# Performance work log

Hardware: AMD Instinct MI355X
Metric: run time of the kernel (lower is better)

Reference implementation:

```python
import jax, jax.numpy as jnp
import numpy as np

B, T, D, H, L, V = 2, 1024, 768, 12, 6, 50257
HS = D // H  # head_size = 64
EPS = 1e-5  # torch LayerNorm default


def _ln(x, g, b):
    m = x.mean(-1, keepdims=True)
    var = ((x - m) ** 2).mean(-1, keepdims=True)
    return (x - m) * jax.lax.rsqrt(var + EPS) * g + b


def setup_inputs() -> dict:
    key = jax.random.key(0)
    ks = jax.random.split(key, 12)
    s = 0.02  # init std per _init_weights
    n = lambda k, shape: jax.random.normal(k, shape, jnp.float32) * s
    return {
        "idx": jax.random.randint(ks[0], (B, T), 0, V),
        "tok_emb": n(ks[1], (V, D)),
        "pos_emb": n(ks[2], (T, D)),
        # per-layer stacked weights; per-head Q/K/V (bias=False in source)
        "wq": n(ks[3], (L, H, D, HS)),
        "wk": n(ks[4], (L, H, D, HS)),
        "wv": n(ks[5], (L, H, D, HS)),
        "wproj": n(ks[6], (L, D, D)),
        "bproj": jnp.zeros((L, D), jnp.float32),
        "w1": n(ks[7], (L, D, 4 * D)),
        "b1": jnp.zeros((L, 4 * D), jnp.float32),
        "w2": n(ks[8], (L, 4 * D, D)),
        "b2": jnp.zeros((L, D), jnp.float32),
        "ln1_g": jnp.ones((L, D), jnp.float32),
        "ln1_b": jnp.zeros((L, D), jnp.float32),
        "ln2_g": jnp.ones((L, D), jnp.float32),
        "ln2_b": jnp.zeros((L, D), jnp.float32),
        "lm_w": n(ks[9], (D, V)),
        "lm_b": jnp.zeros((V,), jnp.float32),
    }


def reference(idx, tok_emb, pos_emb, wq, wk, wv, wproj, bproj, w1, b1, w2,
              b2, ln1_g, ln1_b, ln2_g, ln2_b, lm_w, lm_b):
    x = tok_emb[idx] + pos_emb[None, :, :]  # [B,T,D]
    tril = jnp.tril(jnp.ones((T, T), bool))
    scale = HS ** -0.5  # k.shape[-1] ** -0.5 in source
    for l in range(L):  # small fixed layer count
        # batched per-head QKV (equivalent to the per-head Linear loop + concat)
        q = jnp.einsum('btd,hds->bhts', x, wq[l])
        k = jnp.einsum('btd,hds->bhts', x, wk[l])
        v = jnp.einsum('btd,hds->bhts', x, wv[l])
        wei = jnp.einsum('bhts,bhus->bhtu', q, k) * scale
        wei = jnp.where(tril, wei, -jnp.inf)  # causal forward_mask
        wei = jax.nn.softmax(wei, axis=-1)  # every row has >=1 valid entry
        o = jnp.einsum('bhtu,bhus->bhts', wei, v)
        o = o.transpose(0, 2, 1, 3).reshape(B, T, D)  # concat heads
        sa = o @ wproj[l] + bproj[l]
        x = _ln(x + sa, ln1_g[l], ln1_b[l])  # post-LN as in source
        h = jax.nn.relu(x @ w1[l] + b1[l]) @ w2[l] + b2[l]
        x = _ln(x + h, ln2_g[l], ln2_b[l])
    return x @ lm_w + lm_b  # logits [B,T,V]
```

## Files before the change

### kernel.cpp

```cpp
#include <hip/hip_runtime.h>

#define FLAG_RELU 1
#define FLAG_CAUSAL 2
#define FLAG_OUTF32 4

typedef __attribute__((ext_vector_type(4))) float f32x4;
typedef __attribute__((ext_vector_type(8))) short s16x8;
typedef unsigned short u16;

__device__ __forceinline__ float bf2f(u16 u) {
  union { unsigned int i; float f; } x; x.i = ((unsigned int)u) << 16; return x.f;
}
__device__ __forceinline__ u16 f2bf(float f) {
  union { float f; unsigned int i; } x; x.f = f;
  unsigned int r = (x.i + 0x7fffu + ((x.i >> 16) & 1u)) >> 16;
  return (u16)r;
}

__device__ __forceinline__ void gl_lds16(const u16* g, u16* l) {
  __builtin_amdgcn_global_load_lds(
      (const __attribute__((address_space(1))) unsigned int*)g,
      (__attribute__((address_space(3))) unsigned int*)l, 16, 0, 0);
}

__global__ __launch_bounds__(256) void gemm_bt(
    const u16* __restrict__ A, const u16* __restrict__ Bt, void* __restrict__ Cv,
    int M, int N, int K, int lda, int ldb, int ldc,
    int zdiv, long aS1, long aS2, long bS1, long bS2, long cS1, long cS2,
    const float* __restrict__ bias, float scale, int flags)
{
  __shared__ u16 As[128][32];
  __shared__ u16 Bs[128][32];
  int nx = gridDim.x, ny = gridDim.y;
  int nwg = nx * ny;
  int orig = blockIdx.y * nx + blockIdx.x;
  int q = nwg >> 3, r = nwg & 7;
  int xcd = orig & 7, rest = orig >> 3;
  int wgid = (xcd < r ? xcd * (q + 1) : r * (q + 1) + (xcd - r) * q) + rest;
  int tx = wgid / ny, ty = wgid % ny;

  int z = blockIdx.z;
  int z1 = z / zdiv, z2 = z % zdiv;
  const u16* Ab = A + z1 * aS1 + z2 * aS2 + (long)ty * 128 * lda;
  const u16* Bb = Bt + z1 * bS1 + z2 * bS2 + (long)tx * 128 * ldb;
  long offC = z1 * cS1 + z2 * cS2;
  int tid = threadIdx.x;
  int lane = tid & 63, wave = tid >> 6;
  int wm = (wave >> 1) << 6, wn = (wave & 1) << 6;
  int row0 = tid >> 2, cc = (tid & 3) << 3;
  int fr = lane & 15, fq = (lane >> 4) << 3;
  int m0 = ty * 128, n0 = tx * 128;
  f32x4 acc[4][4] = {};
  bool skip = (flags & FLAG_CAUSAL) && (n0 > m0 + 127);
  if (!skip) {
    const u16* a0p = Ab + (long)row0 * lda + cc;
    const u16* a1p = a0p + 64L * lda;
    const u16* b0p = Bb + (long)row0 * ldb + cc;
    const u16* b1p = b0p + 64L * ldb;
    u16* da0 = &As[0][0] + tid * 8;
    u16* da1 = &As[0][0] + 2048 + tid * 8;
    u16* db0 = &Bs[0][0] + tid * 8;
    u16* db1 = &Bs[0][0] + 2048 + tid * 8;
    for (int k0 = 0; k0 < K; k0 += 32) {
      if (k0) __syncthreads();
      gl_lds16(a0p + k0, da0);
      gl_lds16(a1p + k0, da1);
      gl_lds16(b0p + k0, db0);
      gl_lds16(b1p + k0, db1);
      __syncthreads();
      s16x8 af[4], bfr[4];
#pragma unroll
      for (int i = 0; i < 4; i++) af[i] = *(const s16x8*)&As[wm + i * 16 + fr][fq];
#pragma unroll
      for (int i = 0; i < 4; i++) bfr[i] = *(const s16x8*)&Bs[wn + i * 16 + fr][fq];
#pragma unroll
      for (int mi = 0; mi < 4; mi++)
#pragma unroll
        for (int ni = 0; ni < 4; ni++)
          acc[mi][ni] = __builtin_amdgcn_mfma_f32_16x16x32_bf16(af[mi], bfr[ni], acc[mi][ni], 0, 0, 0);
    }
  }
  int eq = (lane >> 4) << 2;
  float* Cf = (float*)Cv;
  u16* Ch = (u16*)Cv;
#pragma unroll
  for (int ni = 0; ni < 4; ni++) {
    int c = n0 + wn + ni * 16 + fr;
    if (c >= N) continue;
    float bv = bias ? bias[c] : 0.f;
#pragma unroll
    for (int mi = 0; mi < 4; mi++) {
      int rbase = m0 + wm + mi * 16 + eq;
#pragma unroll
      for (int j = 0; j < 4; j++) {
        int r = rbase + j;
        float v = acc[mi][ni][j] * scale + bv;
        if ((flags & FLAG_RELU) && v < 0.f) v = 0.f;
        if ((flags & FLAG_CAUSAL) && c > r) v = -1e30f;
        long idx = offC + (long)r * ldc + c;
        if (flags & FLAG_OUTF32) Cf[idx] = v; else Ch[idx] = f2bf(v);
      }
    }
  }
}

__global__ __launch_bounds__(256) void transpose_f2b(
    const float* __restrict__ src, u16* __restrict__ dst,
    int R, int C, int lds_, int ldd, int Cpad, int zdiv,
    long sS1, long sS2, long dS1, long dS2)
{
  __shared__ u16 tile[32][33];
  int z = blockIdx.z;
  const float* s = src + (z / zdiv) * sS1 + (z % zdiv) * sS2;
  u16* d = dst + (z / zdiv) * dS1 + (z % zdiv) * dS2;
  int c0 = blockIdx.x * 32, r0 = blockIdx.y * 32;
  int tx = threadIdx.x & 31, ty = threadIdx.x >> 5;
#pragma unroll
  for (int i = 0; i < 32; i += 8) {
    int r = r0 + ty + i, c = c0 + tx;
    u16 v = 0;
    if (r < R && c < C) v = f2bf(s[(long)r * lds_ + c]);
    tile[ty + i][tx] = v;
  }
  __syncthreads();
#pragma unroll
  for (int i = 0; i < 32; i += 8) {
    int c = c0 + ty + i, r = r0 + tx;
    if (c < Cpad && r < R) d[(long)c * ldd + r] = tile[tx][ty + i];
  }
}

__global__ __launch_bounds__(256) void transpose_b2b(
    const u16* __restrict__ src, u16* __restrict__ dst,
    int R, int C, int lds_, int ldd, int Cpad, int zdiv,
    long sS1, long sS2, long dS1, long dS2)
{
  __shared__ u16 tile[32][33];
  int z = blockIdx.z;
  const u16* s = src + (z / zdiv) * sS1 + (z % zdiv) * sS2;
  u16* d = dst + (z / zdiv) * dS1 + (z % zdiv) * dS2;
  int c0 = blockIdx.x * 32, r0 = blockIdx.y * 32;
  int tx = threadIdx.x & 31, ty = threadIdx.x >> 5;
#pragma unroll
  for (int i = 0; i < 32; i += 8) {
    int r = r0 + ty + i, c = c0 + tx;
    u16 v = 0;
    if (r < R && c < C) v = s[(long)r * lds_ + c];
    tile[ty + i][tx] = v;
  }
  __syncthreads();
#pragma unroll
  for (int i = 0; i < 32; i += 8) {
    int c = c0 + ty + i, r = r0 + tx;
    if (c < Cpad && r < R) d[(long)c * ldd + r] = tile[tx][ty + i];
  }
}

__global__ __launch_bounds__(256) void softmax_rows(u16* __restrict__ S)
{
  __shared__ float red[8];
  long row = blockIdx.x;
  u16* p = S + row * 1024;
  int tid = threadIdx.x;
  float v[4];
  float mx = -1e30f;
#pragma unroll
  for (int i = 0; i < 4; i++) { v[i] = bf2f(p[tid + i * 256]); mx = fmaxf(mx, v[i]); }
  for (int off = 32; off >= 1; off >>= 1) mx = fmaxf(mx, __shfl_down(mx, off));
  if ((tid & 63) == 0) red[tid >> 6] = mx;
  __syncthreads();
  if (tid == 0) red[4] = fmaxf(fmaxf(red[0], red[1]), fmaxf(red[2], red[3]));
  __syncthreads();
  mx = red[4];
  float sum = 0.f;
#pragma unroll
  for (int i = 0; i < 4; i++) { v[i] = __expf(v[i] - mx); sum += v[i]; }
  for (int off = 32; off >= 1; off >>= 1) sum += __shfl_down(sum, off);
  if ((tid & 63) == 0) red[tid >> 6] = sum;
  __syncthreads();
  if (tid == 0) red[5] = red[0] + red[1] + red[2] + red[3];
  __syncthreads();
  float rs = 1.f / red[5];
#pragma unroll
  for (int i = 0; i < 4; i++) p[tid + i * 256] = f2bf(v[i] * rs);
}

__global__ __launch_bounds__(256) void add_ln(
    float* __restrict__ x, const float* __restrict__ d,
    const float* __restrict__ g, const float* __restrict__ b,
    u16* __restrict__ xb)
{
  __shared__ float red[8];
  long base = blockIdx.x * 768L;
  int tid = threadIdx.x;
  float v[3]; float s = 0.f;
#pragma unroll
  for (int i = 0; i < 3; i++) { int k = tid + i * 256; v[i] = x[base + k] + d[base + k]; s += v[i]; }
  for (int off = 32; off >= 1; off >>= 1) s += __shfl_down(s, off);
  if ((tid & 63) == 0) red[tid >> 6] = s;
  __syncthreads();
  if (tid == 0) red[4] = (red[0] + red[1] + red[2] + red[3]) * (1.f / 768.f);
  __syncthreads();
  float mean = red[4];
  float s2 = 0.f;
#pragma unroll
  for (int i = 0; i < 3; i++) { float t = v[i] - mean; s2 += t * t; }
  for (int off = 32; off >= 1; off >>= 1) s2 += __shfl_down(s2, off);
  if ((tid & 63) == 0) red[tid >> 6] = s2;
  __syncthreads();
  if (tid == 0) red[5] = rsqrtf((red[0] + red[1] + red[2] + red[3]) * (1.f / 768.f) + 1e-5f);
  __syncthreads();
  float rstd = red[5];
#pragma unroll
  for (int i = 0; i < 3; i++) {
    int k = tid + i * 256;
    float y = (v[i] - mean) * rstd * g[k] + b[k];
    x[base + k] = y; xb[base + k] = f2bf(y);
  }
}

__global__ __launch_bounds__(256) void embed_kernel(
    const int* __restrict__ idx, const float* __restrict__ tok, const float* __restrict__ pos,
    float* __restrict__ x, u16* __restrict__ xb)
{
  long row = blockIdx.x;
  int t = (int)(row & 1023);
  long tk = idx[row];
  for (int i = threadIdx.x; i < 768; i += 256) {
    float v = tok[tk * 768 + i] + pos[(long)t * 768 + i];
    x[row * 768 + i] = v;
    xb[row * 768 + i] = f2bf(v);
  }
}

extern "C" void kernel_launch(void* const* d_in, const int* in_sizes, int n_in,
                              void* d_out, int out_size, void* d_ws, size_t ws_size,
                              hipStream_t stream)
{
  const int Bb = 2, T = 1024, D = 768, H = 12, L = 6, V = 50257, HS = 64,
            M = 2048, DFF = 3072, NQ = 2304, VP = 50304;
  const int*   idx     = (const int*)d_in[0];
  const float* tok_emb = (const float*)d_in[1];
  const float* pos_emb = (const float*)d_in[2];
  const float* wq      = (const float*)d_in[3];
  const float* wk      = (const float*)d_in[4];
  const float* wv      = (const float*)d_in[5];
  const float* wproj   = (const float*)d_in[6];
  const float* bproj   = (const float*)d_in[7];
  const float* w1      = (const float*)d_in[8];
  const float* b1      = (const float*)d_in[9];
  const float* w2      = (const float*)d_in[10];
  const float* b2      = (const float*)d_in[11];
  const float* ln1g    = (const float*)d_in[12];
  const float* ln1b    = (const float*)d_in[13];
  const float* ln2g    = (const float*)d_in[14];
  const float* ln2b    = (const float*)d_in[15];
  const float* lmw     = (const float*)d_in[16];
  const float* lmb     = (const float*)d_in[17];
  float* out = (float*)d_out;
  (void)in_sizes; (void)n_in; (void)out_size; (void)ws_size;

  char* ws = (char*)d_ws;
  size_t off = 0;
  auto alloc = [&](size_t bytes) -> char* {
    char* p = ws + off; off += (bytes + 255) & ~(size_t)255; return p;
  };
  u16* wqkv_t  = (u16*)alloc((size_t)L * NQ * D * 2);
  u16* wproj_t = (u16*)alloc((size_t)L * D * D * 2);
  u16* w1_t    = (u16*)alloc((size_t)L * DFF * D * 2);
  u16* w2_t    = (u16*)alloc((size_t)L * D * DFF * 2);
  float* x     = (float*)alloc((size_t)M * D * 4);
  u16* xb      = (u16*)alloc((size_t)M * D * 2);
  char* scratch_base = ws + off;
  u16* qkv     = (u16*)alloc((size_t)M * NQ * 2);
  u16* vt      = (u16*)alloc(((size_t)Bb * H * HS * T + 64 * T) * 2);
  u16* S       = (u16*)alloc((size_t)Bb * H * T * T * 2);
  u16* attn    = (u16*)alloc((size_t)M * D * 2);
  float* tmp   = (float*)alloc((size_t)M * D * 4);
  u16* h1      = (u16*)alloc((size_t)M * DFF * 2);
  u16* lmw_t   = (u16*)scratch_base;

  dim3 blk(256);
  {
    long sS1 = (long)H * D * HS, sS2 = (long)D * HS;
    long dS1 = (long)NQ * D,     dS2 = (long)HS * D;
    transpose_f2b<<<dim3(2, 24, L * H), blk, 0, stream>>>(wq, wqkv_t,                     D, HS, HS, D, HS, H, sS1, sS2, dS1, dS2);
    transpose_f2b<<<dim3(2, 24, L * H), blk, 0, stream>>>(wk, wqkv_t + (size_t)D * D,     D, HS, HS, D, HS, H, sS1, sS2, dS1, dS2);
    transpose_f2b<<<dim3(2, 24, L * H), blk, 0, stream>>>(wv, wqkv_t + (size_t)2 * D * D, D, HS, HS, D, HS, H, sS1, sS2, dS1, dS2);
    transpose_f2b<<<dim3(24, 24, L), blk, 0, stream>>>(wproj, wproj_t, D, D, D, D, D, 1, (long)D * D, 0, (long)D * D, 0);
    transpose_f2b<<<dim3(96, 24, L), blk, 0, stream>>>(w1, w1_t, D, DFF, DFF, D, DFF, 1, (long)D * DFF, 0, (long)DFF * D, 0);
    transpose_f2b<<<dim3(24, 96, L), blk, 0, stream>>>(w2, w2_t, DFF, D, D, DFF, D, 1, (long)DFF * D, 0, (long)D * DFF, 0);
  }
  embed_kernel<<<dim3(M), blk, 0, stream>>>(idx, tok_emb, pos_emb, x, xb);

  for (int l = 0; l < L; l++) {
    gemm_bt<<<dim3(NQ / 128, M / 128, 1), blk, 0, stream>>>(
        xb, wqkv_t + (size_t)l * NQ * D, qkv, M, NQ, D, D, D, NQ,
        1, 0, 0, 0, 0, 0, 0, nullptr, 1.f, 0);
    transpose_b2b<<<dim3(2, 32, Bb * H), blk, 0, stream>>>(
        qkv + 2 * D, vt, T, HS, NQ, T, HS, H,
        (long)T * NQ, (long)HS, (long)H * HS * T, (long)HS * T);
    gemm_bt<<<dim3(T / 128, T / 128, Bb * H), blk, 0, stream>>>(
        qkv, qkv + D, S, T, T, HS, NQ, NQ, T,
        H, (long)T * NQ, (long)HS, (long)T * NQ, (long)HS, (long)H * T * T, (long)T * T,
        nullptr, 0.125f, FLAG_CAUSAL);
    softmax_rows<<<dim3(Bb * H * T), blk, 0, stream>>>(S);
    gemm_bt<<<dim3(1, T / 128, Bb * H), blk, 0, stream>>>(
        S, vt, attn, T, HS, T, T, T, D,
        H, (long)H * T * T, (long)T * T, (long)H * HS * T, (long)HS * T, (long)T * D, (long)HS,
        nullptr, 1.f, 0);
    gemm_bt<<<dim3(D / 128, M / 128, 1), blk, 0, stream>>>(
        attn, wproj_t + (size_t)l * D * D, tmp, M, D, D, D, D, D,
        1, 0, 0, 0, 0, 0, 0, bproj + (size_t)l * D, 1.f, FLAG_OUTF32);
    add_ln<<<dim3(M), blk, 0, stream>>>(x, tmp, ln1g + (size_t)l * D, ln1b + (size_t)l * D, xb);
    gemm_bt<<<dim3(DFF / 128, M / 128, 1), blk, 0, stream>>>(
        xb, w1_t + (size_t)l * DFF * D, h1, M, DFF, D, D, D, DFF,
        1, 0, 0, 0, 0, 0, 0, b1 + (size_t)l * DFF, 1.f, FLAG_RELU);
    gemm_bt<<<dim3(D / 128, M / 128, 1), blk, 0, stream>>>(
        h1, w2_t + (size_t)l * D * DFF, tmp, M, D, DFF, DFF, DFF, D,
        1, 0, 0, 0, 0, 0, 0, b2 + (size_t)l * D, 1.f, FLAG_OUTF32);
    add_ln<<<dim3(M), blk, 0, stream>>>(x, tmp, ln2g + (size_t)l * D, ln2b + (size_t)l * D, xb);
  }
  transpose_f2b<<<dim3(1572, 24, 1), blk, 0, stream>>>(lmw, lmw_t, D, V, V, D, VP, 1, 0, 0, 0, 0);
  gemm_bt<<<dim3(VP / 128, M / 128, 1), blk, 0, stream>>>(
      xb, lmw_t, out, M, V, D, D, D, V,
      1, 0, 0, 0, 0, 0, 0, lmb, 1.f, FLAG_OUTF32);
}
```

Before: 2.521 ms.

## Replace unfused attention with a fused causal flash-attention kernel

Replaces the V transpose, the QK^T GEMM writing a full TxT score matrix, the row softmax and the PV GEMM with a single flash-attention kernel. Each block handles 64 queries of one head, streams 64-key tiles through LDS with online softmax, and skips key tiles above the causal diagonal. This removes the large bf16 score-matrix round trips through global memory and three launches per layer. The trade-off is an unpipelined inner loop with two syncs per tile, a per-element V transpose into LDS, and fairly small blocks.

```diff
diff --git a/kernel.cpp b/kernel.cpp
--- a/kernel.cpp
+++ b/kernel.cpp
@@ -104,6 +104,139 @@
   }
 }
 
+__global__ __launch_bounds__(256) void flash_attn(
+    const u16* __restrict__ qkv, u16* __restrict__ attn)
+{
+  __shared__ u16 QL[4096];
+  __shared__ u16 KL[4096];
+  __shared__ u16 VtL[4096];
+  __shared__ u16 PL[4 * 16 * 72];
+  const int NQ = 2304, D = 768, T = 1024;
+  int qt = blockIdx.x, bh = blockIdx.y;
+  int b = bh / 12, h = bh - b * 12;
+  int q0 = qt * 64;
+  int tid = threadIdx.x;
+  int lane = tid & 63, w = tid >> 6;
+  int fr = lane & 15, g = lane >> 4;
+  int eq = g << 2, fq = g << 3;
+  const u16* base = qkv + (long)(b * T) * NQ + h * 64;
+  const u16* Qg = base + (long)q0 * NQ;
+  const u16* Kg = base + 768;
+  const u16* Vg = base + 1536;
+  int srow = tid >> 2, scol = (tid & 3) << 3;
+  int hs0 = (tid & 3) << 4;
+#pragma unroll
+  for (int c = 0; c < 2; c++)
+    gl_lds16(Qg + (long)srow * NQ + c * 32 + scol, QL + c * 2048 + tid * 8);
+  f32x4 oacc[4] = {};
+  f32x4 m, sml;
+#pragma unroll
+  for (int j = 0; j < 4; j++) { m[j] = -1e30f; sml[j] = 0.f; }
+  int nt = qt + 1;
+  for (int t = 0; t < nt; t++) {
+    const u16* Kt = Kg + (long)(t * 64) * NQ;
+    const u16* Vt = Vg + (long)(t * 64) * NQ;
+    __syncthreads();
+#pragma unroll
+    for (int c = 0; c < 2; c++)
+      gl_lds16(Kt + (long)srow * NQ + c * 32 + scol, KL + c * 2048 + tid * 8);
+    s16x8 v0 = *(const s16x8*)(Vt + (long)srow * NQ + hs0);
+    s16x8 v1 = *(const s16x8*)(Vt + (long)srow * NQ + hs0 + 8);
+    int kc = srow >> 5, kvc = srow & 31;
+#pragma unroll
+    for (int i = 0; i < 16; i++) {
+      u16 val = (u16)(i < 8 ? v0[i] : v1[i - 8]);
+      int hs = hs0 + i;
+      int off = kc * 2048 + hs * 32 + kvc;
+      int byt = (off * 2) ^ (((hs >> 4) & 3) << 4);
+      *(u16*)((char*)VtL + byt) = val;
+    }
+    __syncthreads();
+    f32x4 sf[4] = {};
+#pragma unroll
+    for (int kst = 0; kst < 2; kst++) {
+      s16x8 aq = *(const s16x8*)(QL + kst * 2048 + (w * 16 + fr) * 32 + fq);
+#pragma unroll
+      for (int ni = 0; ni < 4; ni++) {
+        s16x8 bk = *(const s16x8*)(KL + kst * 2048 + (ni * 16 + fr) * 32 + fq);
+        sf[ni] = __builtin_amdgcn_mfma_f32_16x16x32_bf16(aq, bk, sf[ni], 0, 0, 0);
+      }
+    }
+    bool diag = (t == qt);
+#pragma unroll
+    for (int ni = 0; ni < 4; ni++)
+#pragma unroll
+      for (int j = 0; j < 4; j++) {
+        float s = sf[ni][j] * 0.125f;
+        if (diag && (ni * 16 + fr > w * 16 + eq + j)) s = -1e30f;
+        sf[ni][j] = s;
+      }
+    f32x4 rm = sf[0];
+#pragma unroll
+    for (int ni = 1; ni < 4; ni++)
+#pragma unroll
+      for (int j = 0; j < 4; j++) rm[j] = fmaxf(rm[j], sf[ni][j]);
+#pragma unroll
+    for (int o = 1; o <= 8; o <<= 1)
+#pragma unroll
+      for (int j = 0; j < 4; j++) rm[j] = fmaxf(rm[j], __shfl_xor(rm[j], o));
+    f32x4 mn, corr;
+#pragma unroll
+    for (int j = 0; j < 4; j++) {
+      mn[j] = fmaxf(m[j], rm[j]);
+      corr[j] = __expf(m[j] - mn[j]);
+      m[j] = mn[j];
+    }
+    f32x4 rs;
+#pragma unroll
+    for (int j = 0; j < 4; j++) rs[j] = 0.f;
+#pragma unroll
+    for (int ni = 0; ni < 4; ni++)
+#pragma unroll
+      for (int j = 0; j < 4; j++) {
+        float p = __expf(sf[ni][j] - mn[j]);
+        sf[ni][j] = p;
+        rs[j] += p;
+      }
+#pragma unroll
+    for (int o = 1; o <= 8; o <<= 1)
+#pragma unroll
+      for (int j = 0; j < 4; j++) rs[j] += __shfl_xor(rs[j], o);
+#pragma unroll
+    for (int j = 0; j < 4; j++) sml[j] = sml[j] * corr[j] + rs[j];
+#pragma unroll
+    for (int ni = 0; ni < 4; ni++)
+#pragma unroll
+      for (int j = 0; j < 4; j++) oacc[ni][j] *= corr[j];
+    u16* Pw = PL + w * 1152;
+#pragma unroll
+    for (int ni = 0; ni < 4; ni++)
+#pragma unroll
+      for (int j = 0; j < 4; j++)
+        Pw[(eq + j) * 72 + ni * 16 + fr] = f2bf(sf[ni][j]);
+#pragma unroll
+    for (int kst = 0; kst < 2; kst++) {
+      s16x8 ap = *(const s16x8*)(Pw + fr * 72 + kst * 32 + fq);
+#pragma unroll
+      for (int ni = 0; ni < 4; ni++) {
+        int off = kst * 2048 + (ni * 16 + fr) * 32 + fq;
+        int byt = (off * 2) ^ ((ni & 3) << 4);
+        s16x8 bv = *(const s16x8*)((const char*)VtL + byt);
+        oacc[ni] = __builtin_amdgcn_mfma_f32_16x16x32_bf16(ap, bv, oacc[ni], 0, 0, 0);
+      }
+    }
+  }
+  f32x4 rl;
+#pragma unroll
+  for (int j = 0; j < 4; j++) rl[j] = 1.f / sml[j];
+  u16* Og = attn + (long)(b * T + q0 + w * 16) * D + h * 64;
+#pragma unroll
+  for (int ni = 0; ni < 4; ni++)
+#pragma unroll
+    for (int j = 0; j < 4; j++)
+      Og[(long)(eq + j) * D + ni * 16 + fr] = f2bf(oacc[ni][j] * rl[j]);
+}
+
 __global__ __launch_bounds__(256) void transpose_f2b(
     const float* __restrict__ src, u16* __restrict__ dst,
     int R, int C, int lds_, int ldd, int Cpad, int zdiv,
@@ -128,61 +261,6 @@
     int c = c0 + ty + i, r = r0 + tx;
     if (c < Cpad && r < R) d[(long)c * ldd + r] = tile[tx][ty + i];
   }
-}
-
-__global__ __launch_bounds__(256) void transpose_b2b(
-    const u16* __restrict__ src, u16* __restrict__ dst,
-    int R, int C, int lds_, int ldd, int Cpad, int zdiv,
-    long sS1, long sS2, long dS1, long dS2)
-{
-  __shared__ u16 tile[32][33];
-  int z = blockIdx.z;
-  const u16* s = src + (z / zdiv) * sS1 + (z % zdiv) * sS2;
-  u16* d = dst + (z / zdiv) * dS1 + (z % zdiv) * dS2;
-  int c0 = blockIdx.x * 32, r0 = blockIdx.y * 32;
-  int tx = threadIdx.x & 31, ty = threadIdx.x >> 5;
-#pragma unroll
-  for (int i = 0; i < 32; i += 8) {
-    int r = r0 + ty + i, c = c0 + tx;
-    u16 v = 0;
-    if (r < R && c < C) v = s[(long)r * lds_ + c];
-    tile[ty + i][tx] = v;
-  }
-  __syncthreads();
-#pragma unroll
-  for (int i = 0; i < 32; i += 8) {
-    int c = c0 + ty + i, r = r0 + tx;
-    if (c < Cpad && r < R) d[(long)c * ldd + r] = tile[tx][ty + i];
-  }
-}
-
-__global__ __launch_bounds__(256) void softmax_rows(u16* __restrict__ S)
-{
-  __shared__ float red[8];
-  long row = blockIdx.x;
-  u16* p = S + row * 1024;
-  int tid = threadIdx.x;
-  float v[4];
-  float mx = -1e30f;
-#pragma unroll
-  for (int i = 0; i < 4; i++) { v[i] = bf2f(p[tid + i * 256]); mx = fmaxf(mx, v[i]); }
-  for (int off = 32; off >= 1; off >>= 1) mx = fmaxf(mx, __shfl_down(mx, off));
-  if ((tid & 63) == 0) red[tid >> 6] = mx;
-  __syncthreads();
-  if (tid == 0) red[4] = fmaxf(fmaxf(red[0], red[1]), fmaxf(red[2], red[3]));
-  __syncthreads();
-  mx = red[4];
-  float sum = 0.f;
-#pragma unroll
-  for (int i = 0; i < 4; i++) { v[i] = __expf(v[i] - mx); sum += v[i]; }
-  for (int off = 32; off >= 1; off >>= 1) sum += __shfl_down(sum, off);
-  if ((tid & 63) == 0) red[tid >> 6] = sum;
-  __syncthreads();
-  if (tid == 0) red[5] = red[0] + red[1] + red[2] + red[3];
-  __syncthreads();
-  float rs = 1.f / red[5];
-#pragma unroll
-  for (int i = 0; i < 4; i++) p[tid + i * 256] = f2bf(v[i] * rs);
 }
 
 __global__ __launch_bounds__(256) void add_ln(
@@ -273,12 +351,15 @@
   u16* xb      = (u16*)alloc((size_t)M * D * 2);
   char* scratch_base = ws + off;
   u16* qkv     = (u16*)alloc((size_t)M * NQ * 2);
-  u16* vt      = (u16*)alloc(((size_t)Bb * H * HS * T + 64 * T) * 2);
-  u16* S       = (u16*)alloc((size_t)Bb * H * T * T * 2);
   u16* attn    = (u16*)alloc((size_t)M * D * 2);
   float* tmp   = (float*)alloc((size_t)M * D * 4);
   u16* h1      = (u16*)alloc((size_t)M * DFF * 2);
   u16* lmw_t   = (u16*)scratch_base;
+  {
+    size_t scr_off = (size_t)(scratch_base - ws);
+    size_t need = (size_t)VP * D * 2;
+    if (off - scr_off < need) off = scr_off + need;
+  }
 
   dim3 blk(256);
   {
@@ -297,18 +378,7 @@
     gemm_bt<<<dim3(NQ / 128, M / 128, 1), blk, 0, stream>>>(
         xb, wqkv_t + (size_t)l * NQ * D, qkv, M, NQ, D, D, D, NQ,
         1, 0, 0, 0, 0, 0, 0, nullptr, 1.f, 0);
-    transpose_b2b<<<dim3(2, 32, Bb * H), blk, 0, stream>>>(
-        qkv + 2 * D, vt, T, HS, NQ, T, HS, H,
-        (long)T * NQ, (long)HS, (long)H * HS * T, (long)HS * T);
-    gemm_bt<<<dim3(T / 128, T / 128, Bb * H), blk, 0, stream>>>(
-        qkv, qkv + D, S, T, T, HS, NQ, NQ, T,
-        H, (long)T * NQ, (long)HS, (long)T * NQ, (long)HS, (long)H * T * T, (long)T * T,
-        nullptr, 0.125f, FLAG_CAUSAL);
-    softmax_rows<<<dim3(Bb * H * T), blk, 0, stream>>>(S);
-    gemm_bt<<<dim3(1, T / 128, Bb * H), blk, 0, stream>>>(
-        S, vt, attn, T, HS, T, T, T, D,
-        H, (long)H * T * T, (long)T * T, (long)H * HS * T, (long)HS * T, (long)T * D, (long)HS,
-        nullptr, 1.f, 0);
+    flash_attn<<<dim3(T / 64, Bb * H), blk, 0, stream>>>(qkv, attn);
     gemm_bt<<<dim3(D / 128, M / 128, 1), blk, 0, stream>>>(
         attn, wproj_t + (size_t)l * D * D, tmp, M, D, D, D, D, D,
         1, 0, 0, 0, 0, 0, 0, bproj + (size_t)l * D, 1.f, FLAG_OUTF32);
```

New measurement: 2.253 ms. 10.6% less time.
